# Kernel tuning notes

Measured on AMD Instinct MI355X. Metric: run time of the kernel, lower is better.

## Reference

```python
import jax, jax.numpy as jnp
import numpy as np

N_NODES = 100000

def gcn_conv(x, W, b, src, dst, n_nodes):
    # x: [N, Fin], W: [Fin, Fout], b: [Fout]; src/dst include self-loops.
    h = x @ W                                            # [N, Fout]
    deg = jnp.zeros((n_nodes,), x.dtype).at[dst].add(1.0)  # in-degree incl. self-loop
    dinv = jax.lax.rsqrt(deg)                            # deg >= 1 due to self-loops
    norm = dinv[src] * dinv[dst]                         # [E']
    msg = h[src] * norm[:, None]                         # [E', Fout]
    out = jax.ops.segment_sum(msg, dst, num_segments=n_nodes)
    return out + b

def setup_inputs() -> dict:
    key = jax.random.key(0)
    k1, k2, k3, k4, k5, k6 = jax.random.split(key, 6)
    in_c, hid_c, out_c = 128, 64, 32
    x = jax.random.normal(k1, (N_NODES, in_c), dtype=jnp.float32)
    edge_index = jax.random.randint(k2, (2, 1600000), 0, N_NODES, dtype=jnp.int64)
    # Glorot-ish init for weights
    W1 = jax.random.normal(k3, (in_c, hid_c), dtype=jnp.float32) / np.sqrt(in_c)
    b1 = jnp.zeros((hid_c,), dtype=jnp.float32)
    W2 = jax.random.normal(k4, (hid_c, out_c), dtype=jnp.float32) / np.sqrt(hid_c)
    b2 = jnp.zeros((out_c,), dtype=jnp.float32)
    return {"x": x, "edge_index": edge_index, "W1": W1, "b1": b1, "W2": W2, "b2": b2}

def reference(x, edge_index, W1, b1, W2, b2):
    n = x.shape[0]
    loops = jnp.arange(n, dtype=edge_index.dtype)
    src = jnp.concatenate([edge_index[0], loops])   # add self-loops
    dst = jnp.concatenate([edge_index[1], loops])
    h = gcn_conv(x, W1, b1, src, dst, n)
    h = jax.nn.relu(h)
    out = gcn_conv(h, W2, b2, src, dst, n)
    return out
```

## Files before the change

kernel.cpp:

```cpp
#include <hip/hip_runtime.h>
#include <hip/hip_bf16.h>


#define FIN1 128
#define FOUT1 64
#define FOUT2 32
#define PAD 64
#define NPB 200
#define NBUCKET 500
#define CAP 4096
#define EPB 4096

typedef unsigned int uint;
typedef unsigned short ushort;
typedef __attribute__((ext_vector_type(8))) short bf16x8;
typedef __attribute__((ext_vector_type(4))) float f32x4;

__device__ __forceinline__ ushort f2bf(float f) {
    uint u = __float_as_uint(f);
    return (ushort)((u + 0x7fffu + ((u >> 16) & 1u)) >> 16);
}
__device__ __forceinline__ float bf2f(ushort b) {
    return __uint_as_float(((uint)b) << 16);
}


__global__ __launch_bounds__(256) void bin_edges(const int* __restrict__ src,
                                                 const int* __restrict__ dst,
                                                 int* __restrict__ cursors,
                                                 int* __restrict__ binned, int e) {
    __shared__ int s_hist[NBUCKET];
    __shared__ int s_base[NBUCKET];
    __shared__ int s_cur[NBUCKET];
    const int t = threadIdx.x;
    for (int i = t; i < NBUCKET; i += 256) s_hist[i] = 0;
    __syncthreads();
    const int base = blockIdx.x * EPB;
    int vpk[16], vb[16];
#pragma unroll
    for (int k = 0; k < 16; ++k) {
        int idx = base + t + k * 256;
        bool ok = idx < e;
        int s = ok ? src[idx] : 0;
        int d = ok ? dst[idx] : 0;
        int bk = d / NPB;
        vb[k] = ok ? bk : -1;
        vpk[k] = s | ((d - bk * NPB) << 17);
        if (ok) atomicAdd(&s_hist[bk], 1);
    }
    __syncthreads();
    for (int i = t; i < NBUCKET; i += 256) {
        int h = s_hist[i];
        s_base[i] = (h > 0) ? atomicAdd(&cursors[i], h) : 0;
        s_cur[i] = 0;
    }
    __syncthreads();
#pragma unroll
    for (int k = 0; k < 16; ++k) {
        int bk = vb[k];
        if (bk >= 0) {
            int r = s_base[bk] + atomicAdd(&s_cur[bk], 1);
            if (r < CAP) binned[(size_t)bk * CAP + r] = vpk[k];
        }
    }
}


__global__ __launch_bounds__(256) void build_ell(const int* __restrict__ binned,
                                                 const int* __restrict__ cursors,
                                                 int* __restrict__ counts,
                                                 float* __restrict__ dinv,
                                                 int* __restrict__ ell, int n) {
    __shared__ int s_cnt[NPB];
    __shared__ int s_ell[NPB * PAD];
    const int b = blockIdx.x, t = threadIdx.x;
    for (int i = t; i < NPB; i += 256) s_cnt[i] = 0;
    __syncthreads();
    const int len = min(cursors[b], CAP);
    const int* edges = binned + (size_t)b * CAP;
    const int node0 = b * NPB;
    for (int i = t; i < len; i += 256) {
        int pk = edges[i];
        int local = pk >> 17;
        int r = atomicAdd(&s_cnt[local], 1);
        if (r < PAD) s_ell[local * PAD + r] = pk & 0x1FFFF;
    }
    __syncthreads();
    for (int i = t; i < NPB; i += 256) {
        int node = node0 + i;
        if (node < n) {
            int full = s_cnt[i];
            counts[node] = min(full, PAD);
            dinv[node] = rsqrtf((float)full + 1.0f);
        }
    }
    int4* d4 = (int4*)(ell + (size_t)node0 * PAD);
    const int4* s4 = (const int4*)s_ell;
    for (int i = t; i < NPB * PAD / 4; i += 256) d4[i] = s4[i];
}


template <int K, int F, bool ABF>
__global__ __launch_bounds__(256) void gemm_mfma(const void* __restrict__ Av,
                                                 const float* __restrict__ W,
                                                 const float* __restrict__ dinv,
                                                 ushort* __restrict__ out, int n) {
    constexpr int KC = K / 32;
    constexpr int CT = F / 16;
    constexpr int CSH = (CT == 4) ? 2 : 1;
    __shared__ ushort sB[KC * CT * 64 * 8];
    const int t = threadIdx.x;
    for (int d = t; d < K * F; d += 256) {
        int j = d & 7;
        int ln = (d >> 3) & 63;
        int c = (d >> 9) & (CT - 1);
        int kc = d >> (9 + CSH);
        int k = kc * 32 + (ln >> 4) * 8 + j;
        int f = c * 16 + (ln & 15);
        sB[d] = f2bf(W[(size_t)k * F + f]);
    }
    __syncthreads();

    const int w = threadIdx.x >> 6;
    const int lane = threadIdx.x & 63;
    const int quad = lane >> 4;
    const int mcol = lane & 15;

    bf16x8 bfr[KC][CT];
    const bf16x8* sB8 = reinterpret_cast<const bf16x8*>(sB);
#pragma unroll
    for (int kc = 0; kc < KC; ++kc)
#pragma unroll
        for (int c = 0; c < CT; ++c)
            bfr[kc][c] = sB8[(kc * CT + c) * 64 + lane];

    const int ntiles = n / 16;
#pragma unroll
    for (int tt = 0; tt < 2; ++tt) {
        const int tile = (blockIdx.x * 4 + w) * 2 + tt;
        if (tile >= ntiles) continue;
        const int rb = tile * 16;
        bf16x8 afr[KC];
#pragma unroll
        for (int kc = 0; kc < KC; ++kc) {
            if (ABF) {
                const ushort* ap = (const ushort*)Av + (size_t)(rb + mcol) * K + kc * 32 + quad * 8;
                afr[kc] = *reinterpret_cast<const bf16x8*>(ap);
            } else {
                const float* ap = (const float*)Av + (size_t)(rb + mcol) * K + kc * 32 + quad * 8;
                float4 x0 = *reinterpret_cast<const float4*>(ap);
                float4 x1 = *reinterpret_cast<const float4*>(ap + 4);
                bf16x8 a;
                a[0] = (short)f2bf(x0.x); a[1] = (short)f2bf(x0.y);
                a[2] = (short)f2bf(x0.z); a[3] = (short)f2bf(x0.w);
                a[4] = (short)f2bf(x1.x); a[5] = (short)f2bf(x1.y);
                a[6] = (short)f2bf(x1.z); a[7] = (short)f2bf(x1.w);
                afr[kc] = a;
            }
        }
        f32x4 acc[CT];
#pragma unroll
        for (int c = 0; c < CT; ++c) acc[c] = (f32x4){0.f, 0.f, 0.f, 0.f};
#pragma unroll
        for (int kc = 0; kc < KC; ++kc)
#pragma unroll
            for (int c = 0; c < CT; ++c)
                acc[c] = __builtin_amdgcn_mfma_f32_16x16x32_bf16(afr[kc], bfr[kc][c], acc[c], 0, 0, 0);
        float dv[4];
#pragma unroll
        for (int r = 0; r < 4; ++r) dv[r] = dinv[rb + quad * 4 + r];
#pragma unroll
        for (int c = 0; c < CT; ++c)
#pragma unroll
            for (int r = 0; r < 4; ++r)
                out[(size_t)(rb + quad * 4 + r) * F + c * 16 + mcol] = f2bf(acc[c][r] * dv[r]);
    }
}


__global__ __launch_bounds__(256) void aggregate64_bf(const ushort* __restrict__ h,
                                                      const int* __restrict__ counts,
                                                      const int* __restrict__ ell,
                                                      const float* __restrict__ dinv,
                                                      const float* __restrict__ bias,
                                                      ushort* __restrict__ out, int n) {
    const int wv = __builtin_amdgcn_readfirstlane(threadIdx.x >> 6);
    const int node = blockIdx.x * 4 + wv;
    const int lane = threadIdx.x & 63;
    if (node >= n) return;
    const int cnt = counts[node];
    const int* __restrict__ row = ell + (size_t)node * PAD;
    float acc = bf2f(h[(size_t)node * 64 + lane]);
    int r = 0;
    for (; r + 16 <= cnt; r += 16) {
        float v[16];
#pragma unroll
        for (int i = 0; i < 16; ++i) v[i] = bf2f(h[(size_t)row[r + i] * 64 + lane]);
        float t0 = ((v[0] + v[1]) + (v[2] + v[3])) + ((v[4] + v[5]) + (v[6] + v[7]));
        float t1 = ((v[8] + v[9]) + (v[10] + v[11])) + ((v[12] + v[13]) + (v[14] + v[15]));
        acc += t0 + t1;
    }
    for (; r + 8 <= cnt; r += 8) {
        float v[8];
#pragma unroll
        for (int i = 0; i < 8; ++i) v[i] = bf2f(h[(size_t)row[r + i] * 64 + lane]);
        acc += ((v[0] + v[1]) + (v[2] + v[3])) + ((v[4] + v[5]) + (v[6] + v[7]));
    }
    for (; r + 4 <= cnt; r += 4) {
        float v[4];
#pragma unroll
        for (int i = 0; i < 4; ++i) v[i] = bf2f(h[(size_t)row[r + i] * 64 + lane]);
        acc += (v[0] + v[1]) + (v[2] + v[3]);
    }
    for (; r < cnt; ++r) acc += bf2f(h[(size_t)row[r] * 64 + lane]);
    float v = fmaxf(acc * dinv[node] + bias[lane], 0.0f);
    out[(size_t)node * 64 + lane] = f2bf(v);
}

__global__ __launch_bounds__(256) void aggregate32_bf(const ushort* __restrict__ h,
                                                      const int* __restrict__ counts,
                                                      const int* __restrict__ ell,
                                                      const float* __restrict__ dinv,
                                                      const float* __restrict__ bias,
                                                      float* __restrict__ out, int n) {
    const int wv = __builtin_amdgcn_readfirstlane(threadIdx.x >> 6);
    const int node = blockIdx.x * 4 + wv;
    const int lane = threadIdx.x & 63;
    const int f = lane & 31;
    if (node >= n) return;
    const int cnt = counts[node];
    const int* __restrict__ row = ell + (size_t)node * PAD;
    float acc = bf2f(h[(size_t)node * 32 + f]);
    int r = 0;
    for (; r + 16 <= cnt; r += 16) {
        float v[16];
#pragma unroll
        for (int i = 0; i < 16; ++i) v[i] = bf2f(h[(size_t)row[r + i] * 32 + f]);
        float t0 = ((v[0] + v[1]) + (v[2] + v[3])) + ((v[4] + v[5]) + (v[6] + v[7]));
        float t1 = ((v[8] + v[9]) + (v[10] + v[11])) + ((v[12] + v[13]) + (v[14] + v[15]));
        acc += t0 + t1;
    }
    for (; r + 8 <= cnt; r += 8) {
        float v[8];
#pragma unroll
        for (int i = 0; i < 8; ++i) v[i] = bf2f(h[(size_t)row[r + i] * 32 + f]);
        acc += ((v[0] + v[1]) + (v[2] + v[3])) + ((v[4] + v[5]) + (v[6] + v[7]));
    }
    for (; r + 4 <= cnt; r += 4) {
        float v[4];
#pragma unroll
        for (int i = 0; i < 4; ++i) v[i] = bf2f(h[(size_t)row[r + i] * 32 + f]);
        acc += (v[0] + v[1]) + (v[2] + v[3]);
    }
    for (; r < cnt; ++r) acc += bf2f(h[(size_t)row[r] * 32 + f]);
    float v = acc * dinv[node] + bias[f];
    if (lane < 32) out[(size_t)node * 32 + f] = v;
}

extern "C" void kernel_launch(void* const* d_in, const int* in_sizes, int n_in,
                              void* d_out, int out_size, void* d_ws, size_t ws_size,
                              hipStream_t stream) {
    const float* x  = (const float*)d_in[0];
    const int*   ei = (const int*)d_in[1];
    const float* W1 = (const float*)d_in[2];
    const float* b1 = (const float*)d_in[3];
    const float* W2 = (const float*)d_in[4];
    const float* b2 = (const float*)d_in[5];
    float* out = (float*)d_out;

    const int N = in_sizes[0] / FIN1;
    const int E = in_sizes[1] / 2;
    const int* src = ei;
    const int* dst = ei + E;

    char* w = (char*)d_ws;
    size_t off = 0;
    auto alloc = [&](size_t bytes) -> char* {
        char* p = w + off;
        off = (off + bytes + 255) & ~(size_t)255;
        return p;
    };
    int*    cursors = (int*)alloc((size_t)NBUCKET * 4);
    int*    counts  = (int*)alloc((size_t)N * 4);
    float*  dinv    = (float*)alloc((size_t)N * 4);
    int*    binned  = (int*)alloc((size_t)NBUCKET * CAP * 4);
    int*    ell     = (int*)alloc((size_t)N * PAD * 4);
    ushort* hbf     = (ushort*)alloc((size_t)N * 64 * 2);
    ushort* h1bf    = (ushort*)alloc((size_t)N * 64 * 2);
    (void)ws_size;

    const int BINB = (E + EPB - 1) / EPB;
    const int GB = (N / 16 + 7) / 8;
    const int AB = (N + 3) / 4;

    hipMemsetAsync(cursors, 0, (size_t)NBUCKET * 4, stream);
    bin_edges<<<BINB, 256, 0, stream>>>(src, dst, cursors, binned, E);
    build_ell<<<NBUCKET, 256, 0, stream>>>(binned, cursors, counts, dinv, ell, N);

    gemm_mfma<FIN1, FOUT1, false><<<GB, 256, 0, stream>>>(x, W1, dinv, hbf, N);
    aggregate64_bf<<<AB, 256, 0, stream>>>(hbf, counts, ell, dinv, b1, h1bf, N);

    gemm_mfma<FOUT1, FOUT2, true><<<GB, 256, 0, stream>>>(h1bf, W2, dinv, hbf, N);
    aggregate32_bf<<<AB, 256, 0, stream>>>(hbf, counts, ell, dinv, b2, out, N);
}
```

Measured before the change: 234.9 us.

## Fuse layer-1 aggregation with layer-2 GEMM through shared-memory tile

Merges the 64-wide neighbor aggregation and the second GEMM into one kernel. Each block aggregates 16 nodes into an LDS tile, then two waves run MFMA against staged W2. This removes the h1 round-trip through global memory and one launch. W staging is also rewritten so global reads of W are coalesced. In exchange, each block restages W2, only two waves do the MFMA, and each wave handles 4 nodes serially, which may reduce latency hiding in the gather. It also assumes N is a multiple of 16.

```diff
diff --git a/kernel.cpp b/kernel.cpp
--- a/kernel.cpp
+++ b/kernel.cpp
@@ -99,26 +99,29 @@
     for (int i = t; i < NPB * PAD / 4; i += 256) d4[i] = s4[i];
 }
 
-
-template <int K, int F, bool ABF>
-__global__ __launch_bounds__(256) void gemm_mfma(const void* __restrict__ Av,
+template <int K, int F, int CT, int LOG2F>
+__device__ __forceinline__ void stage_W(const float* __restrict__ W, ushort* sB, int t) {
+    for (int sidx = t; sidx < K * F; sidx += 256) {
+        int k = sidx >> LOG2F;
+        int f = sidx & (F - 1);
+        int kc = k >> 5, j = k & 7, quadb = (k >> 3) & 3;
+        int c = f >> 4, nn = f & 15;
+        int d = ((kc * CT + c) * 64 + quadb * 16 + nn) * 8 + j;
+        sB[d] = f2bf(W[sidx]);
+    }
+}
+
+
+template <int K, int F, int LOG2F>
+__global__ __launch_bounds__(256) void gemm_mfma(const float* __restrict__ A,
                                                  const float* __restrict__ W,
                                                  const float* __restrict__ dinv,
                                                  ushort* __restrict__ out, int n) {
     constexpr int KC = K / 32;
     constexpr int CT = F / 16;
-    constexpr int CSH = (CT == 4) ? 2 : 1;
     __shared__ ushort sB[KC * CT * 64 * 8];
     const int t = threadIdx.x;
-    for (int d = t; d < K * F; d += 256) {
-        int j = d & 7;
-        int ln = (d >> 3) & 63;
-        int c = (d >> 9) & (CT - 1);
-        int kc = d >> (9 + CSH);
-        int k = kc * 32 + (ln >> 4) * 8 + j;
-        int f = c * 16 + (ln & 15);
-        sB[d] = f2bf(W[(size_t)k * F + f]);
-    }
+    stage_W<K, F, CT, LOG2F>(W, sB, t);
     __syncthreads();
 
     const int w = threadIdx.x >> 6;
@@ -143,20 +146,15 @@
         bf16x8 afr[KC];
 #pragma unroll
         for (int kc = 0; kc < KC; ++kc) {
-            if (ABF) {
-                const ushort* ap = (const ushort*)Av + (size_t)(rb + mcol) * K + kc * 32 + quad * 8;
-                afr[kc] = *reinterpret_cast<const bf16x8*>(ap);
-            } else {
-                const float* ap = (const float*)Av + (size_t)(rb + mcol) * K + kc * 32 + quad * 8;
-                float4 x0 = *reinterpret_cast<const float4*>(ap);
-                float4 x1 = *reinterpret_cast<const float4*>(ap + 4);
-                bf16x8 a;
-                a[0] = (short)f2bf(x0.x); a[1] = (short)f2bf(x0.y);
-                a[2] = (short)f2bf(x0.z); a[3] = (short)f2bf(x0.w);
-                a[4] = (short)f2bf(x1.x); a[5] = (short)f2bf(x1.y);
-                a[6] = (short)f2bf(x1.z); a[7] = (short)f2bf(x1.w);
-                afr[kc] = a;
-            }
+            const float* ap = A + (size_t)(rb + mcol) * K + kc * 32 + quad * 8;
+            float4 x0 = *reinterpret_cast<const float4*>(ap);
+            float4 x1 = *reinterpret_cast<const float4*>(ap + 4);
+            bf16x8 a;
+            a[0] = (short)f2bf(x0.x); a[1] = (short)f2bf(x0.y);
+            a[2] = (short)f2bf(x0.z); a[3] = (short)f2bf(x0.w);
+            a[4] = (short)f2bf(x1.x); a[5] = (short)f2bf(x1.y);
+            a[6] = (short)f2bf(x1.z); a[7] = (short)f2bf(x1.w);
+            afr[kc] = a;
         }
         f32x4 acc[CT];
 #pragma unroll
@@ -178,44 +176,77 @@
 }
 
 
-__global__ __launch_bounds__(256) void aggregate64_bf(const ushort* __restrict__ h,
-                                                      const int* __restrict__ counts,
-                                                      const int* __restrict__ ell,
-                                                      const float* __restrict__ dinv,
-                                                      const float* __restrict__ bias,
-                                                      ushort* __restrict__ out, int n) {
-    const int wv = __builtin_amdgcn_readfirstlane(threadIdx.x >> 6);
-    const int node = blockIdx.x * 4 + wv;
-    const int lane = threadIdx.x & 63;
-    if (node >= n) return;
-    const int cnt = counts[node];
-    const int* __restrict__ row = ell + (size_t)node * PAD;
-    float acc = bf2f(h[(size_t)node * 64 + lane]);
-    int r = 0;
-    for (; r + 16 <= cnt; r += 16) {
-        float v[16];
-#pragma unroll
-        for (int i = 0; i < 16; ++i) v[i] = bf2f(h[(size_t)row[r + i] * 64 + lane]);
-        float t0 = ((v[0] + v[1]) + (v[2] + v[3])) + ((v[4] + v[5]) + (v[6] + v[7]));
-        float t1 = ((v[8] + v[9]) + (v[10] + v[11])) + ((v[12] + v[13]) + (v[14] + v[15]));
-        acc += t0 + t1;
-    }
-    for (; r + 8 <= cnt; r += 8) {
-        float v[8];
-#pragma unroll
-        for (int i = 0; i < 8; ++i) v[i] = bf2f(h[(size_t)row[r + i] * 64 + lane]);
-        acc += ((v[0] + v[1]) + (v[2] + v[3])) + ((v[4] + v[5]) + (v[6] + v[7]));
-    }
-    for (; r + 4 <= cnt; r += 4) {
-        float v[4];
-#pragma unroll
-        for (int i = 0; i < 4; ++i) v[i] = bf2f(h[(size_t)row[r + i] * 64 + lane]);
-        acc += (v[0] + v[1]) + (v[2] + v[3]);
-    }
-    for (; r < cnt; ++r) acc += bf2f(h[(size_t)row[r] * 64 + lane]);
-    float v = fmaxf(acc * dinv[node] + bias[lane], 0.0f);
-    out[(size_t)node * 64 + lane] = f2bf(v);
-}
+#define SASTRIDE 72
+
+__global__ __launch_bounds__(256) void agg_gemm2(const ushort* __restrict__ h,
+                                                 const int* __restrict__ counts,
+                                                 const int* __restrict__ ell,
+                                                 const float* __restrict__ dinv,
+                                                 const float* __restrict__ bias,
+                                                 const float* __restrict__ W2,
+                                                 ushort* __restrict__ out, int n) {
+    constexpr int KC = 2;
+    constexpr int CT = 2;
+    __shared__ ushort sB[KC * CT * 64 * 8];
+    __shared__ ushort sA[16 * SASTRIDE];
+    const int t = threadIdx.x;
+    stage_W<64, 32, CT, 5>(W2, sB, t);
+
+    const int w = __builtin_amdgcn_readfirstlane(t >> 6);
+    const int lane = t & 63;
+    const int rb = blockIdx.x * 16;
+
+    for (int i = 0; i < 4; ++i) {
+        const int node = rb + w * 4 + i;
+        const int cnt = counts[node];
+        const int* __restrict__ row = ell + (size_t)node * PAD;
+        float acc = bf2f(h[(size_t)node * 64 + lane]);
+        int r = 0;
+        for (; r + 16 <= cnt; r += 16) {
+            float v[16];
+#pragma unroll
+            for (int u = 0; u < 16; ++u) v[u] = bf2f(h[(size_t)row[r + u] * 64 + lane]);
+            float t0 = ((v[0] + v[1]) + (v[2] + v[3])) + ((v[4] + v[5]) + (v[6] + v[7]));
+            float t1 = ((v[8] + v[9]) + (v[10] + v[11])) + ((v[12] + v[13]) + (v[14] + v[15]));
+            acc += t0 + t1;
+        }
+        for (; r + 8 <= cnt; r += 8) {
+            float v[8];
+#pragma unroll
+            for (int u = 0; u < 8; ++u) v[u] = bf2f(h[(size_t)row[r + u] * 64 + lane]);
+            acc += ((v[0] + v[1]) + (v[2] + v[3])) + ((v[4] + v[5]) + (v[6] + v[7]));
+        }
+        for (; r + 4 <= cnt; r += 4) {
+            float v[4];
+#pragma unroll
+            for (int u = 0; u < 4; ++u) v[u] = bf2f(h[(size_t)row[r + u] * 64 + lane]);
+            acc += (v[0] + v[1]) + (v[2] + v[3]);
+        }
+        for (; r < cnt; ++r) acc += bf2f(h[(size_t)row[r] * 64 + lane]);
+        float v = fmaxf(acc * dinv[node] + bias[lane], 0.0f);
+        sA[(w * 4 + i) * SASTRIDE + lane] = f2bf(v);
+    }
+    __syncthreads();
+
+    if (w < 2) {
+        const int quad = lane >> 4;
+        const int mcol = lane & 15;
+        const bf16x8* sB8 = reinterpret_cast<const bf16x8*>(sB);
+        f32x4 acc = (f32x4){0.f, 0.f, 0.f, 0.f};
+#pragma unroll
+        for (int kc = 0; kc < KC; ++kc) {
+            bf16x8 afr = *reinterpret_cast<const bf16x8*>(&sA[mcol * SASTRIDE + kc * 32 + quad * 8]);
+            bf16x8 bfr = sB8[(kc * CT + w) * 64 + lane];
+            acc = __builtin_amdgcn_mfma_f32_16x16x32_bf16(afr, bfr, acc, 0, 0, 0);
+        }
+#pragma unroll
+        for (int r = 0; r < 4; ++r) {
+            int orow = rb + quad * 4 + r;
+            out[(size_t)orow * 32 + w * 16 + mcol] = f2bf(acc[r] * dinv[orow]);
+        }
+    }
+}
+
 
 __global__ __launch_bounds__(256) void aggregate32_bf(const ushort* __restrict__ h,
                                                       const int* __restrict__ counts,
@@ -286,20 +317,19 @@
     int*    binned  = (int*)alloc((size_t)NBUCKET * CAP * 4);
     int*    ell     = (int*)alloc((size_t)N * PAD * 4);
     ushort* hbf     = (ushort*)alloc((size_t)N * 64 * 2);
-    ushort* h1bf    = (ushort*)alloc((size_t)N * 64 * 2);
+    ushort* h2bf    = (ushort*)alloc((size_t)N * 32 * 2);
     (void)ws_size;
 
     const int BINB = (E + EPB - 1) / EPB;
     const int GB = (N / 16 + 7) / 8;
+    const int FB = N / 16;
     const int AB = (N + 3) / 4;
 
     hipMemsetAsync(cursors, 0, (size_t)NBUCKET * 4, stream);
     bin_edges<<<BINB, 256, 0, stream>>>(src, dst, cursors, binned, E);
     build_ell<<<NBUCKET, 256, 0, stream>>>(binned, cursors, counts, dinv, ell, N);
 
-    gemm_mfma<FIN1, FOUT1, false><<<GB, 256, 0, stream>>>(x, W1, dinv, hbf, N);
-    aggregate64_bf<<<AB, 256, 0, stream>>>(hbf, counts, ell, dinv, b1, h1bf, N);
-
-    gemm_mfma<FOUT1, FOUT2, true><<<GB, 256, 0, stream>>>(h1bf, W2, dinv, hbf, N);
-    aggregate32_bf<<<AB, 256, 0, stream>>>(hbf, counts, ell, dinv, b2, out, N);
-}
+    gemm_mfma<FIN1, FOUT1, 6><<<GB, 256, 0, stream>>>(x, W1, dinv, hbf, N);
+    agg_gemm2<<<FB, 256, 0, stream>>>(hbf, counts, ell, dinv, b1, W2, h2bf, N);
+    aggregate32_bf<<<AB, 256, 0, stream>>>(h2bf, counts, ell, dinv, b2, out, N);
+}
```

Result: faster. 229.9 us (-2.1%).
